# Optimization experiments

Measured on AMD Instinct MI355X. Metric: run time of the kernel, lower is better.

Reference implementation:

```python
import jax, jax.numpy as jnp
import numpy as np

WINDOW = 11
C1 = 0.01 ** 2
C2 = 0.03 ** 2
PAD = WINDOW // 2


def _box_filter(img, kernel):
    # img: [B,1,H,W], kernel: [1,1,w,w]; SAME padding (odd window)
    return jax.lax.conv_general_dilated(
        img, kernel,
        window_strides=(1, 1),
        padding=[(PAD, PAD), (PAD, PAD)],
        dimension_numbers=('NCHW', 'OIHW', 'NCHW'))


def setup_inputs() -> dict:
    key = jax.random.key(0)
    kx, ky = jax.random.split(key)
    B, C, H, W = 64, 1, 512, 512
    x = jax.random.uniform(kx, (B, C, H, W), dtype=jnp.float32)
    y = jax.random.uniform(ky, (B, C, H, W), dtype=jnp.float32)
    kernel = jnp.ones((1, 1, WINDOW, WINDOW), dtype=jnp.float32) / (WINDOW ** 2)
    return {"x": x, "y": y, "kernel": kernel}


def reference(x, y, kernel):
    mu_x = _box_filter(x, kernel)
    mu_y = _box_filter(y, kernel)
    mu_x2 = mu_x * mu_x
    mu_y2 = mu_y * mu_y
    mu_xy = mu_x * mu_y
    sigma_x2 = _box_filter(x * x, kernel) - mu_x2
    sigma_y2 = _box_filter(y * y, kernel) - mu_y2
    sigma_xy = _box_filter(x * y, kernel) - mu_xy
    ssim_map = ((2.0 * mu_xy + C1) * (2.0 * sigma_xy + C2)) / (
        (mu_x2 + mu_y2 + C1) * (sigma_x2 + sigma_y2 + C2))
    return 1.0 - jnp.mean(ssim_map)
```

## Files before the change

### kernel.cpp

```cpp
#include <hip/hip_runtime.h>
#include <stdint.h>


#define IMG_H 512
#define IMG_W 512
#define N_IMG 64
#define RAD   5
#define SH    16
#define NBANDG 8
#define NBLOCKS (N_IMG * NBANDG)

#define C1_SSIM 1.0e-4f
#define C2_SSIM 9.0e-4f

#define SLOT_BYTES 4096

typedef __attribute__((address_space(3))) uint32_t lds_u32_t;
typedef const __attribute__((address_space(1))) uint32_t glb_u32_t;

__device__ __forceinline__ void dma16(void* lds, const void* g) {
    __builtin_amdgcn_global_load_lds((glb_u32_t*)g, (lds_u32_t*)lds, 16, 0, 0);
}

__device__ __forceinline__ float dpp_up1(float v) {
    int r = __builtin_amdgcn_update_dpp(0, __float_as_int(v), 0x138, 0xf, 0xf, true);
    return __int_as_float(r);
}
__device__ __forceinline__ float dpp_dn1(float v) {
    int r = __builtin_amdgcn_update_dpp(0, __float_as_int(v), 0x130, 0xf, 0xf, true);
    return __int_as_float(r);
}

__global__ __launch_bounds__(256) void ssim_fused(const float* __restrict__ x,
                                                  const float* __restrict__ y,
                                                  float* __restrict__ part)
{
    __shared__ __align__(16) char ring[4][2][SLOT_BYTES];

    const int tx  = threadIdx.x & 63;
    const int ts  = threadIdx.x >> 6;
    const int img = blockIdx.x >> 3;
    const int bg  = blockIdx.x & (NBANDG - 1);
    const int r0  = bg * (4 * SH) + ts * SH;
    const int c0  = tx * 8;

    const float* __restrict__ xi = x + (size_t)img * (IMG_H * IMG_W);
    const float* __restrict__ yi = y + (size_t)img * (IMG_H * IMG_W);

    auto dma_row = [&](char* s, int ri) -> float {
        int rc = ri < 0 ? 0 : (ri > IMG_H - 1 ? IMG_H - 1 : ri);
        float sc = (ri >= 0 && ri < IMG_H) ? 1.0f : 0.0f;
        const char* xg = (const char*)(xi + (size_t)rc * IMG_W) + tx * 16;
        const char* yg = (const char*)(yi + (size_t)rc * IMG_W) + tx * 16;
        dma16(s,        xg);
        dma16(s + 1024, xg + 1024);
        dma16(s + 2048, yg);
        dma16(s + 3072, yg + 1024);
        return sc;
    };

    float Vx[8], Vy[8], Vxx[8], Vyy[8], Vxy[8];
#pragma unroll
    for (int j = 0; j < 8; ++j) { Vx[j] = 0.f; Vy[j] = 0.f; Vxx[j] = 0.f; Vyy[j] = 0.f; Vxy[j] = 0.f; }

    auto accum_lds = [&](const char* s, float f) {
        const float4* xr = (const float4*)(s + (size_t)tx * 32);
        const float4* yr = (const float4*)(s + 2048 + (size_t)tx * 32);
        float4 x0 = xr[0], x1 = xr[1];
        float4 y0 = yr[0], y1 = yr[1];
        float xs[8] = {x0.x, x0.y, x0.z, x0.w, x1.x, x1.y, x1.z, x1.w};
        float ys[8] = {y0.x, y0.y, y0.z, y0.w, y1.x, y1.y, y1.z, y1.w};
#pragma unroll
        for (int j = 0; j < 8; ++j) {
            float fx = f * xs[j];
            float fy = f * ys[j];
            Vx[j] += fx;
            Vy[j] += fy;
            Vxx[j] = fmaf(fx, xs[j], Vxx[j]);
            Vyy[j] = fmaf(fy, ys[j], Vyy[j]);
            Vxy[j] = fmaf(fx, ys[j], Vxy[j]);
        }
    };

    auto hsum = [&](const float (&V)[8], float (&S)[8]) {
        float w[18];
#pragma unroll
        for (int k = 0; k < 5; ++k) w[k] = dpp_up1(V[3 + k]);
#pragma unroll
        for (int j = 0; j < 8; ++j) w[5 + j] = V[j];
#pragma unroll
        for (int k = 0; k < 5; ++k) w[13 + k] = dpp_dn1(V[k]);
        float s = 0.f;
#pragma unroll
        for (int t = 0; t < 11; ++t) s += w[t];
        S[0] = s;
#pragma unroll
        for (int j = 1; j < 8; ++j) { s += w[j + 10] - w[j - 1]; S[j] = s; }
    };

    char* cur = &ring[ts][0][0];
    char* nxt = &ring[ts][1][0];

    float scCur = dma_row(cur, r0 - 5);
#pragma unroll 1
    for (int i = 0; i < 2 * RAD; ++i) {
        accum_lds(cur, scCur);
        float scN = dma_row(nxt, r0 - 4 + i);
        char* t = cur; cur = nxt; nxt = t;
        scCur = scN;
    }

    const float inv121 = 1.0f / 121.0f;
    float loss = 0.0f;

#pragma unroll 1
    for (int ro = r0; ro < r0 + SH; ++ro) {
        accum_lds(cur, scCur);
        float scN = dma_row(nxt, ro + 6);

        int  rs      = ro - RAD;
        bool haveSub = (rs >= 0);
        float4 sx0, sx1, sy0, sy1;
        if (haveSub) {
            const float4* xr = (const float4*)(xi + (size_t)rs * IMG_W + c0);
            const float4* yr = (const float4*)(yi + (size_t)rs * IMG_W + c0);
            sx0 = xr[0]; sx1 = xr[1]; sy0 = yr[0]; sy1 = yr[1];
        }

        float Sx[8], Sy[8], Sxx[8], Syy[8], Sxy[8];
        hsum(Vx,  Sx);
        hsum(Vy,  Sy);
        hsum(Vxx, Sxx);
        hsum(Vyy, Syy);
        hsum(Vxy, Sxy);

#pragma unroll
        for (int j = 0; j < 8; ++j) {
            float mx  = Sx[j] * inv121;
            float my  = Sy[j] * inv121;
            float mx2 = mx * mx;
            float my2 = my * my;
            float mxy = mx * my;
            float vx  = Sxx[j] * inv121 - mx2;
            float vy  = Syy[j] * inv121 - my2;
            float vxy = Sxy[j] * inv121 - mxy;
            float num = (2.0f * mxy + C1_SSIM) * (2.0f * vxy + C2_SSIM);
            float den = (mx2 + my2 + C1_SSIM) * (vx + vy + C2_SSIM);
            loss += __fdividef(num, den);
        }

        if (haveSub) {
            float xs[8] = {sx0.x, sx0.y, sx0.z, sx0.w, sx1.x, sx1.y, sx1.z, sx1.w};
            float ys[8] = {sy0.x, sy0.y, sy0.z, sy0.w, sy1.x, sy1.y, sy1.z, sy1.w};
#pragma unroll
            for (int j = 0; j < 8; ++j) {
                Vx[j]  -= xs[j];
                Vy[j]  -= ys[j];
                Vxx[j] = fmaf(-xs[j], xs[j], Vxx[j]);
                Vyy[j] = fmaf(-ys[j], ys[j], Vyy[j]);
                Vxy[j] = fmaf(-xs[j], ys[j], Vxy[j]);
            }
        }

        char* t = cur; cur = nxt; nxt = t;
        scCur = scN;
    }

#pragma unroll
    for (int off = 32; off > 0; off >>= 1)
        loss += __shfl_down(loss, off, 64);

    __shared__ float pr[4];
    if (tx == 0) pr[ts] = loss;
    __syncthreads();
    if (threadIdx.x == 0)
        part[blockIdx.x] = (pr[0] + pr[1]) + (pr[2] + pr[3]);
}

__global__ __launch_bounds__(256) void ssim_reduce(const float* __restrict__ part,
                                                   float* __restrict__ out)
{
    const int t  = threadIdx.x;
    const int tx = t & 63;
    float s = part[t] + part[t + 256];
#pragma unroll
    for (int off = 32; off > 0; off >>= 1)
        s += __shfl_down(s, off, 64);
    __shared__ float ws[4];
    if (tx == 0) ws[t >> 6] = s;
    __syncthreads();
    if (t == 0) {
        float total = (ws[0] + ws[1]) + (ws[2] + ws[3]);
        out[0] = 1.0f - total * (1.0f / ((float)N_IMG * IMG_H * IMG_W));
    }
}

extern "C" void kernel_launch(void* const* d_in, const int* in_sizes, int n_in,
                              void* d_out, int out_size, void* d_ws, size_t ws_size,
                              hipStream_t stream) {
    const float* x = (const float*)d_in[0];
    const float* y = (const float*)d_in[1];
    float* part = (float*)d_ws;

    ssim_fused<<<NBLOCKS, 256, 0, stream>>>(x, y, part);
    ssim_reduce<<<1, 256, 0, stream>>>(part, (float*)d_out);
}
```

Before: 173.9 us.

## Use one wave per block with a deep LDS ring buffer and taller strips

Each block becomes a single 64-thread wave that processes a 64-row strip, so the 10-row halo is amortised over more output rows. A 14-slot LDS ring lets rows be DMA-prefetched several iterations ahead. The subtracted row is now read back from the ring instead of being reloaded from global memory. The cost is fewer waves in flight (512 waves total), more LDS per block, and a reliance on per-wave DMA ordering without explicit waits. This may limit latency hiding and occupancy.

```diff
diff --git a/kernel.cpp b/kernel.cpp
--- a/kernel.cpp
+++ b/kernel.cpp
@@ -6,14 +6,16 @@
 #define IMG_W 512
 #define N_IMG 64
 #define RAD   5
-#define SH    16
-#define NBANDG 8
-#define NBLOCKS (N_IMG * NBANDG)
+#define SH    64
+#define NSTRIP 8
+#define NBLOCKS (N_IMG * NSTRIP)
 
 #define C1_SSIM 1.0e-4f
 #define C2_SSIM 9.0e-4f
 
 #define SLOT_BYTES 4096
+#define RING_SLOTS 14
+#define RING_BYTES (RING_SLOTS * SLOT_BYTES)
 
 typedef __attribute__((address_space(3))) uint32_t lds_u32_t;
 typedef const __attribute__((address_space(1))) uint32_t glb_u32_t;
@@ -31,54 +33,59 @@
     return __int_as_float(r);
 }
 
-__global__ __launch_bounds__(256) void ssim_fused(const float* __restrict__ x,
-                                                  const float* __restrict__ y,
-                                                  float* __restrict__ part)
+__global__ __launch_bounds__(64) void ssim_fused(const float* __restrict__ x,
+                                                 const float* __restrict__ y,
+                                                 float* __restrict__ part)
 {
-    __shared__ __align__(16) char ring[4][2][SLOT_BYTES];
+    __shared__ __align__(16) char ring[RING_BYTES];
 
-    const int tx  = threadIdx.x & 63;
-    const int ts  = threadIdx.x >> 6;
+    const int tx  = threadIdx.x;
     const int img = blockIdx.x >> 3;
-    const int bg  = blockIdx.x & (NBANDG - 1);
-    const int r0  = bg * (4 * SH) + ts * SH;
-    const int c0  = tx * 8;
+    const int st  = blockIdx.x & (NSTRIP - 1);
+    const int r0  = st * SH;
 
     const float* __restrict__ xi = x + (size_t)img * (IMG_H * IMG_W);
     const float* __restrict__ yi = y + (size_t)img * (IMG_H * IMG_W);
 
-    auto dma_row = [&](char* s, int ri) -> float {
-        int rc = ri < 0 ? 0 : (ri > IMG_H - 1 ? IMG_H - 1 : ri);
-        float sc = (ri >= 0 && ri < IMG_H) ? 1.0f : 0.0f;
-        const char* xg = (const char*)(xi + (size_t)rc * IMG_W) + tx * 16;
-        const char* yg = (const char*)(yi + (size_t)rc * IMG_W) + tx * 16;
+    auto dma_row = [&](int so, int ri) {
+        const char* xg = (const char*)(xi + (size_t)ri * IMG_W) + tx * 16;
+        const char* yg = (const char*)(yi + (size_t)ri * IMG_W) + tx * 16;
+        char* s = ring + so;
         dma16(s,        xg);
         dma16(s + 1024, xg + 1024);
         dma16(s + 2048, yg);
         dma16(s + 3072, yg + 1024);
-        return sc;
     };
 
     float Vx[8], Vy[8], Vxx[8], Vyy[8], Vxy[8];
 #pragma unroll
     for (int j = 0; j < 8; ++j) { Vx[j] = 0.f; Vy[j] = 0.f; Vxx[j] = 0.f; Vyy[j] = 0.f; Vxy[j] = 0.f; }
 
-    auto accum_lds = [&](const char* s, float f) {
-        const float4* xr = (const float4*)(s + (size_t)tx * 32);
-        const float4* yr = (const float4*)(s + 2048 + (size_t)tx * 32);
+    auto accum_lds = [&](int so, bool add) {
+        const float4* xr = (const float4*)(ring + so + (size_t)tx * 32);
+        const float4* yr = (const float4*)(ring + so + 2048 + (size_t)tx * 32);
         float4 x0 = xr[0], x1 = xr[1];
         float4 y0 = yr[0], y1 = yr[1];
         float xs[8] = {x0.x, x0.y, x0.z, x0.w, x1.x, x1.y, x1.z, x1.w};
         float ys[8] = {y0.x, y0.y, y0.z, y0.w, y1.x, y1.y, y1.z, y1.w};
+        if (add) {
 #pragma unroll
-        for (int j = 0; j < 8; ++j) {
-            float fx = f * xs[j];
-            float fy = f * ys[j];
-            Vx[j] += fx;
-            Vy[j] += fy;
-            Vxx[j] = fmaf(fx, xs[j], Vxx[j]);
-            Vyy[j] = fmaf(fy, ys[j], Vyy[j]);
-            Vxy[j] = fmaf(fx, ys[j], Vxy[j]);
+            for (int j = 0; j < 8; ++j) {
+                Vx[j]  += xs[j];
+                Vy[j]  += ys[j];
+                Vxx[j] = fmaf(xs[j], xs[j], Vxx[j]);
+                Vyy[j] = fmaf(ys[j], ys[j], Vyy[j]);
+                Vxy[j] = fmaf(xs[j], ys[j], Vxy[j]);
+            }
+        } else {
+#pragma unroll
+            for (int j = 0; j < 8; ++j) {
+                Vx[j]  -= xs[j];
+                Vy[j]  -= ys[j];
+                Vxx[j] = fmaf(-xs[j], xs[j], Vxx[j]);
+                Vyy[j] = fmaf(-ys[j], ys[j], Vyy[j]);
+                Vxy[j] = fmaf(-xs[j], ys[j], Vxy[j]);
+            }
         }
     };
 
@@ -98,34 +105,30 @@
         for (int j = 1; j < 8; ++j) { s += w[j + 10] - w[j - 1]; S[j] = s; }
     };
 
-    char* cur = &ring[ts][0][0];
-    char* nxt = &ring[ts][1][0];
+#pragma unroll
+    for (int i = 0; i < 13; ++i) {
+        int ri = r0 - 5 + i;
+        if (ri >= 0 && ri < IMG_H) dma_row(i * SLOT_BYTES, ri);
+    }
+#pragma unroll 1
+    for (int i = 0; i < 10; ++i) {
+        int ri = r0 - 5 + i;
+        if (ri >= 0) accum_lds(i * SLOT_BYTES, true);
+    }
 
-    float scCur = dma_row(cur, r0 - 5);
-#pragma unroll 1
-    for (int i = 0; i < 2 * RAD; ++i) {
-        accum_lds(cur, scCur);
-        float scN = dma_row(nxt, r0 - 4 + i);
-        char* t = cur; cur = nxt; nxt = t;
-        scCur = scN;
-    }
+    int subOff = 0;
+    int addOff = 10 * SLOT_BYTES;
+    int dmaOff = 13 * SLOT_BYTES;
 
     const float inv121 = 1.0f / 121.0f;
     float loss = 0.0f;
 
 #pragma unroll 1
     for (int ro = r0; ro < r0 + SH; ++ro) {
-        accum_lds(cur, scCur);
-        float scN = dma_row(nxt, ro + 6);
+        if (ro + RAD < IMG_H) accum_lds(addOff, true);
 
-        int  rs      = ro - RAD;
-        bool haveSub = (rs >= 0);
-        float4 sx0, sx1, sy0, sy1;
-        if (haveSub) {
-            const float4* xr = (const float4*)(xi + (size_t)rs * IMG_W + c0);
-            const float4* yr = (const float4*)(yi + (size_t)rs * IMG_W + c0);
-            sx0 = xr[0]; sx1 = xr[1]; sy0 = yr[0]; sy1 = yr[1];
-        }
+        int rd = ro + 8;
+        if (rd < IMG_H && rd <= r0 + SH + 4) dma_row(dmaOff, rd);
 
         float Sx[8], Sy[8], Sxx[8], Syy[8], Sxy[8];
         hsum(Vx,  Sx);
@@ -149,32 +152,17 @@
             loss += __fdividef(num, den);
         }
 
-        if (haveSub) {
-            float xs[8] = {sx0.x, sx0.y, sx0.z, sx0.w, sx1.x, sx1.y, sx1.z, sx1.w};
-            float ys[8] = {sy0.x, sy0.y, sy0.z, sy0.w, sy1.x, sy1.y, sy1.z, sy1.w};
-#pragma unroll
-            for (int j = 0; j < 8; ++j) {
-                Vx[j]  -= xs[j];
-                Vy[j]  -= ys[j];
-                Vxx[j] = fmaf(-xs[j], xs[j], Vxx[j]);
-                Vyy[j] = fmaf(-ys[j], ys[j], Vyy[j]);
-                Vxy[j] = fmaf(-xs[j], ys[j], Vxy[j]);
-            }
-        }
+        if (ro - RAD >= 0) accum_lds(subOff, false);
 
-        char* t = cur; cur = nxt; nxt = t;
-        scCur = scN;
+        subOff += SLOT_BYTES; if (subOff == RING_BYTES) subOff = 0;
+        addOff += SLOT_BYTES; if (addOff == RING_BYTES) addOff = 0;
+        dmaOff += SLOT_BYTES; if (dmaOff == RING_BYTES) dmaOff = 0;
     }
 
 #pragma unroll
     for (int off = 32; off > 0; off >>= 1)
         loss += __shfl_down(loss, off, 64);
-
-    __shared__ float pr[4];
-    if (tx == 0) pr[ts] = loss;
-    __syncthreads();
-    if (threadIdx.x == 0)
-        part[blockIdx.x] = (pr[0] + pr[1]) + (pr[2] + pr[3]);
+    if (tx == 0) part[blockIdx.x] = loss;
 }
 
 __global__ __launch_bounds__(256) void ssim_reduce(const float* __restrict__ part,
@@ -202,6 +190,6 @@
     const float* y = (const float*)d_in[1];
     float* part = (float*)d_ws;
 
-    ssim_fused<<<NBLOCKS, 256, 0, stream>>>(x, y, part);
+    ssim_fused<<<NBLOCKS, 64, 0, stream>>>(x, y, part);
     ssim_reduce<<<1, 256, 0, stream>>>(part, (float*)d_out);
 }
```

New measurement: 208.9 us. +20.1%, slower.
